# Kernel tuning notes

Measured on AMD Instinct MI355X. Metric: run time of the kernel, lower is better.

## Reference

```python
import jax, jax.numpy as jnp
import numpy as np
from jax import lax

B, T, E, H, D, L = 2048, 512, 128, 8, 16, 3


def _ln(x, g, b):
    m = jnp.mean(x, -1, keepdims=True)
    v = jnp.var(x, -1, keepdims=True)
    return (x - m) / jnp.sqrt(v + 1e-5) * g + b


def _bn(x, g, b):  # eval-mode BatchNorm2d with running_mean=0, running_var=1
    return x * (g / np.sqrt(1.0 + 1e-5))[None, :, None, None] + b[None, :, None, None]


def _conv(x, w, b):  # 3x3 conv, padding=1, NCHW / OIHW
    y = lax.conv_general_dilated(x, w, (1, 1), 'SAME', dimension_numbers=('NCHW', 'OIHW', 'NCHW'))
    return y + b[None, :, None, None]


def _forward(enc_out, x1, x2, x3, c11_w, c11_b, bn11_g, bn11_b, c12_w, c12_b, bn12_g, bn12_b,
             fc1_w, fc1_b, c21_w, c21_b, bn21_g, bn21_b, fc2_w, fc2_b, fc_w, fc_b,
             wk, wq, wv, proj_w, proj_b, ln1_g, ln1_b, ln2_g, ln2_b, ln3_g, ln3_b, ln4_g, ln4_b,
             ff_w1, ff_b1, ff_w2, ff_b2, lnf_g, lnf_b, head_w, head_b):
    # StateNet -> query vector q: [B, E]
    h1 = jax.nn.relu(_bn(_conv(x1, c11_w, c11_b), bn11_g, bn11_b))
    h1 = jax.nn.relu(_bn(_conv(h1, c12_w, c12_b), bn12_g, bn12_b))
    h1 = jax.nn.relu(h1.reshape(h1.shape[0], -1) @ fc1_w + fc1_b)  # [B, 64]
    h2 = jax.nn.relu(_bn(_conv(x2, c21_w, c21_b), bn21_g, bn21_b))
    h2 = jax.nn.relu(h2.reshape(h2.shape[0], -1) @ fc2_w + fc2_b)  # [B, 16]
    q = jax.nn.relu(jnp.concatenate([h1, h2, x3], axis=-1) @ fc_w + fc_b)  # [B, E]

    for l in range(L):  # 3 structurally identical DecoderBlocks
        kx = _ln(enc_out, ln1_g[l], ln1_b[l])
        vx = _ln(enc_out, ln2_g[l], ln2_b[l])
        qx = _ln(q, ln3_g[l], ln3_b[l])
        K = (kx @ wk[l]).reshape(B, T, H, D)
        V = (vx @ wv[l]).reshape(B, T, H, D)
        Q = (qx @ wq[l]).reshape(B, H, D)
        # NOTE: original multiplies (not divides) by head_size**0.5 -- kept faithful.
        wei = jax.nn.softmax(jnp.einsum('bhd,bthd->bht', Q, K) * (D ** 0.5), axis=-1)
        att = jnp.einsum('bht,bthd->bhd', wei, V).reshape(B, E)
        q = q + att @ proj_w[l] + proj_b[l]
        h = _ln(q, ln4_g[l], ln4_b[l])
        q = q + jax.nn.gelu(h @ ff_w1[l] + ff_b1[l], approximate=False) @ ff_w2[l] + ff_b2[l]

    x = _ln(q, lnf_g, lnf_b)
    return x @ head_w + head_b  # discard head logits [B, 37]


def setup_inputs():
    key = jax.random.key(0)
    ks = iter(jax.random.split(key, 32))
    r = lambda *s: jax.random.normal(next(ks), s, jnp.float32) * 0.02
    z = lambda *s: jnp.zeros(s, jnp.float32)
    o = lambda *s: jnp.ones(s, jnp.float32)
    return dict(
        enc_out=jax.random.normal(next(ks), (B, T, E), jnp.float32),
        x1=jax.random.normal(next(ks), (B, 3, 37, 1), jnp.float32),
        x2=jax.random.normal(next(ks), (B, 7, 4, 1), jnp.float32),
        x3=jax.random.normal(next(ks), (B, 4), jnp.float32),
        c11_w=r(8, 3, 3, 3), c11_b=z(8), bn11_g=o(8), bn11_b=z(8),
        c12_w=r(8, 8, 3, 3), c12_b=z(8), bn12_g=o(8), bn12_b=z(8),
        fc1_w=r(296, 64), fc1_b=z(64),
        c21_w=r(8, 7, 3, 3), c21_b=z(8), bn21_g=o(8), bn21_b=z(8),
        fc2_w=r(32, 16), fc2_b=z(16),
        fc_w=r(84, E), fc_b=z(E),
        wk=r(L, E, E), wq=r(L, E, E), wv=r(L, E, E),
        proj_w=r(L, E, E), proj_b=z(L, E),
        ln1_g=o(L, E), ln1_b=z(L, E), ln2_g=o(L, E), ln2_b=z(L, E),
        ln3_g=o(L, E), ln3_b=z(L, E), ln4_g=o(L, E), ln4_b=z(L, E),
        ff_w1=r(L, E, 4 * E), ff_b1=z(L, 4 * E), ff_w2=r(L, 4 * E, E), ff_b2=z(L, E),
        lnf_g=o(E), lnf_b=z(E),
        head_w=r(E, 37), head_b=z(37),
    )


def reference(enc_out, x1, x2, x3, c11_w, c11_b, bn11_g, bn11_b, c12_w, c12_b, bn12_g, bn12_b,
              fc1_w, fc1_b, c21_w, c21_b, bn21_g, bn21_b, fc2_w, fc2_b, fc_w, fc_b,
              wk, wq, wv, proj_w, proj_b, ln1_g, ln1_b, ln2_g, ln2_b, ln3_g, ln3_b, ln4_g, ln4_b,
              ff_w1, ff_b1, ff_w2, ff_b2, lnf_g, lnf_b, head_w, head_b):
    return _forward(enc_out, x1, x2, x3, c11_w, c11_b, bn11_g, bn11_b, c12_w, c12_b, bn12_g, bn12_b,
                    fc1_w, fc1_b, c21_w, c21_b, bn21_g, bn21_b, fc2_w, fc2_b, fc_w, fc_b,
                    wk, wq, wv, proj_w, proj_b, ln1_g, ln1_b, ln2_g, ln2_b, ln3_g, ln3_b, ln4_g, ln4_b,
                    ff_w1, ff_b1, ff_w2, ff_b2, lnf_g, lnf_b, head_w, head_b)
```

## Files before the change

kernel.cpp:

```cpp
#include <hip/hip_runtime.h>
#include <math.h>

typedef unsigned int u32;
typedef unsigned short u16;
typedef unsigned char u8;
typedef __attribute__((ext_vector_type(4))) float f32x4;
typedef __attribute__((ext_vector_type(8))) short bf16x8;

__device__ __forceinline__ u16 f2b(float f){ u32 u=__float_as_uint(f); u=(u+0x7fffu+((u>>16)&1u))>>16; return (u16)u; }
__device__ __forceinline__ float b2f(u16 h){ return __uint_as_float(((u32)h)<<16); }

struct P {
  const float* in[43];
  float* out;
  float* q;
};

__global__ __launch_bounds__(512) void k_state(P p){
  __shared__ float sx1[112];
  __shared__ float sx2[32];
  __shared__ float sa[296];
  __shared__ float sb[296];
  __shared__ float sc2[32];
  __shared__ float sh1[64];
  __shared__ float sh2[16];
  __shared__ float red[512];
  int tid=threadIdx.x; int b=blockIdx.x;
  const float rs_bn = rsqrtf(1.0f+1e-5f);
  const float* x1 = p.in[1] + (size_t)b*111;
  const float* x2 = p.in[2] + (size_t)b*28;
  if (tid<111) sx1[tid]=x1[tid];
  if (tid>=128 && tid<156) sx2[tid-128]=x2[tid-128];
  __syncthreads();
  if (tid<296){
    int cc=tid/37, i=tid-cc*37;
    const float* wgt=p.in[4];
    float acc=p.in[5][cc];
    #pragma unroll
    for(int ic=0;ic<3;++ic)
      #pragma unroll
      for(int kh=0;kh<3;++kh){
        int ii=i+kh-1;
        if((unsigned)ii<37u) acc+=wgt[((cc*3+ic)*3+kh)*3+1]*sx1[ic*37+ii];
      }
    acc=acc*(p.in[6][cc]*rs_bn)+p.in[7][cc];
    sa[tid]=fmaxf(acc,0.f);
  }
  if (tid>=296 && tid<328){
    int o=tid-296, cc=o>>2, i=o&3;
    const float* wgt=p.in[14];
    float acc=p.in[15][cc];
    for(int ic=0;ic<7;++ic)
      for(int kh=0;kh<3;++kh){
        int ii=i+kh-1;
        if((unsigned)ii<4u) acc+=wgt[((cc*7+ic)*3+kh)*3+1]*sx2[ic*4+ii];
      }
    acc=acc*(p.in[16][cc]*rs_bn)+p.in[17][cc];
    sc2[o]=fmaxf(acc,0.f);
  }
  __syncthreads();
  if (tid<296){
    int cc=tid/37, i=tid-cc*37;
    const float* wgt=p.in[8];
    float acc=p.in[9][cc];
    #pragma unroll
    for(int ic=0;ic<8;++ic)
      #pragma unroll
      for(int kh=0;kh<3;++kh){
        int ii=i+kh-1;
        if((unsigned)ii<37u) acc+=wgt[((cc*8+ic)*3+kh)*3+1]*sa[ic*37+ii];
      }
    acc=acc*(p.in[10][cc]*rs_bn)+p.in[11][cc];
    sb[tid]=fmaxf(acc,0.f);
  }
  if (tid>=480 && tid<496){
    int o=tid-480;
    const float* wgt=p.in[18];
    float acc=p.in[19][o];
    for(int k=0;k<32;++k) acc+=sc2[k]*wgt[k*16+o];
    sh2[o]=fmaxf(acc,0.f);
  }
  __syncthreads();
  {
    int o=tid>>3, j=tid&7;
    const float* wgt=p.in[12];
    float part=0.f;
    for(int m=0;m<37;++m){ int k=j*37+m; part+=sb[k]*wgt[k*64+o]; }
    red[o*8+j]=part;
  }
  __syncthreads();
  if (tid<64){
    float acc=p.in[13][tid];
    #pragma unroll
    for(int j=0;j<8;++j) acc+=red[tid*8+j];
    sh1[tid]=fmaxf(acc,0.f);
  }
  __syncthreads();
  if (tid<128){
    const float* wgt=p.in[20];
    const float* x3=p.in[3]+(size_t)b*4;
    float acc=p.in[21][tid];
    for(int k=0;k<64;++k) acc+=sh1[k]*wgt[k*128+tid];
    for(int k=0;k<16;++k) acc+=sh2[k]*wgt[(64+k)*128+tid];
    #pragma unroll
    for(int k=0;k<4;++k) acc+=x3[k]*wgt[(80+k)*128+tid];
    p.q[(size_t)b*128+tid]=fmaxf(acc,0.f);
  }
}

#define FUSED_LDS 157184

__global__ __launch_bounds__(512,1) void k_fused(P p){
  extern __shared__ u8 sm[];
  u16*  XH   = (u16*)sm;
  u8*   WTU  = sm + 139264;
  float* qv   = (float*)(sm + 155904);
  float* wred = (float*)(sm + 156416);
  float* mrow = (float*)(sm + 156928);
  float* invL = (float*)(sm + 156992);
  float* st   = (float*)(sm + 157056);

  float* red  = (float*)(WTU);
  float* qxs  = (float*)(WTU + 2048);
  float* Qs   = (float*)(WTU + 2560);
  u16*  QKb   = (u16*)(WTU + 3072);
  u16*  WT    = (u16*)(WTU);
  float* SS   = (float*)(WTU);
  float* red2 = (float*)(WTU + 4224);
  float* atts = (float*)(WTU + 6272);
  float* qps  = (float*)(WTU + 6784);
  float* qx4  = (float*)(WTU + 7296);
  float* us   = (float*)(WTU + 7808);

  int tid=threadIdx.x;
  int w = tid>>6, lane = tid&63, l15 = lane&15, q4 = lane>>4;
  int b = blockIdx.x;

  {
    const float* enc = p.in[0] + (size_t)b*512*128;
    int g = tid>>5, c = tid&31;
    #pragma unroll 4
    for (int it=0; it<32; ++it){
      int row = it*16 + g;
      float4 v = *(const float4*)(enc + (size_t)row*128 + c*4);
      float s = v.x+v.y+v.z+v.w;
      float s2 = v.x*v.x+v.y*v.y+v.z*v.z+v.w*v.w;
      #pragma unroll
      for (int m=1; m<=16; m<<=1){ s+=__shfl_xor(s,m); s2+=__shfl_xor(s2,m); }
      float mean = s*(1.f/128.f);
      float rstd = rsqrtf(s2*(1.f/128.f)-mean*mean+1e-5f);
      u32 a = (u32)f2b((v.x-mean)*rstd) | ((u32)f2b((v.y-mean)*rstd)<<16);
      u32 bq= (u32)f2b((v.z-mean)*rstd) | ((u32)f2b((v.w-mean)*rstd)<<16);
      *(uint2*)(XH + row*136 + c*4) = make_uint2(a,bq);
    }
    if (tid<128) qv[tid] = p.q[(size_t)b*128 + tid];
  }
  __syncthreads();

  for (int l=0; l<3; ++l){
    const float* wk = p.in[22] + l*16384;
    const float* wq = p.in[23] + l*16384;
    const float* wv = p.in[24] + l*16384;
    const float* pw = p.in[25] + l*16384;
    const float* pb = p.in[26] + l*128;
    const float* g1 = p.in[27] + l*128;
    const float* g2 = p.in[29] + l*128;
    const float* b2v= p.in[30] + l*128;
    const float* g3 = p.in[31] + l*128;
    const float* b3 = p.in[32] + l*128;
    const float* g4 = p.in[33] + l*128;
    const float* b4 = p.in[34] + l*128;
    const float* f1 = p.in[35] + l*65536;
    const float* fb1= p.in[36] + l*512;
    const float* f2 = p.in[37] + l*65536;
    const float* fb2= p.in[38] + l*128;

    if (w==0){
      float x0=qv[lane], x1=qv[lane+64];
      float s=x0+x1, s2=x0*x0+x1*x1;
      #pragma unroll
      for(int m=1;m<=32;m<<=1){ s+=__shfl_xor(s,m); s2+=__shfl_xor(s2,m); }
      if(lane==0){ float mean=s*(1.f/128.f); st[0]=mean; st[1]=rsqrtf(s2*(1.f/128.f)-mean*mean+1e-5f); }
    }
    __syncthreads();
    if (tid<128) qxs[tid]=(qv[tid]-st[0])*st[1]*g3[tid]+b3[tid];
    __syncthreads();

    {
      int o = tid&127, kk = tid>>7;
      float acc=0.f;
      const float* wp = wq + kk*32*128 + o;
      #pragma unroll 8
      for (int e=0;e<32;++e) acc += qxs[kk*32+e]*wp[e*128];
      red[tid]=acc;
    }
    __syncthreads();
    if (tid<128) Qs[tid]=red[tid]+red[tid+128]+red[tid+256]+red[tid+384];
    __syncthreads();

    {
      int h = tid>>5, e0=(tid&31)*4;
      if (h<8){
        float Qh[16];
        #pragma unroll
        for(int d=0;d<16;++d) Qh[d]=Qs[h*16+d];
        #pragma unroll
        for(int j=0;j<4;++j){
          int e=e0+j;
          const float* wr = wk + e*128 + h*16;
          float4 wv0=*(const float4*)(wr), wv1=*(const float4*)(wr+4), wv2=*(const float4*)(wr+8), wv3=*(const float4*)(wr+12);
          float acc = Qh[0]*wv0.x+Qh[1]*wv0.y+Qh[2]*wv0.z+Qh[3]*wv0.w
                    + Qh[4]*wv1.x+Qh[5]*wv1.y+Qh[6]*wv1.z+Qh[7]*wv1.w
                    + Qh[8]*wv2.x+Qh[9]*wv2.y+Qh[10]*wv2.z+Qh[11]*wv2.w
                    + Qh[12]*wv3.x+Qh[13]*wv3.y+Qh[14]*wv3.z+Qh[15]*wv3.w;
          QKb[h*136+e] = f2b(acc*g1[e]*4.f);
        }
      } else {
        #pragma unroll
        for(int j=0;j<4;++j) QKb[h*136+e0+j]=0;
      }
    }
    __syncthreads();

    bf16x8 qkf[4];
    #pragma unroll
    for(int ks=0;ks<4;++ks) qkf[ks]=*(const bf16x8*)(QKb + l15*136 + ks*32 + q4*8);

    f32x4 sc[4];
    #pragma unroll
    for(int mb=0;mb<4;++mb){
      f32x4 c = {0.f,0.f,0.f,0.f};
      #pragma unroll
      for(int ks=0;ks<4;++ks){
        bf16x8 a = *(const bf16x8*)(XH + (64*w + 16*mb + l15)*136 + ks*32 + q4*8);
        c = __builtin_amdgcn_mfma_f32_16x16x32_bf16(a, qkf[ks], c, 0,0,0);
      }
      sc[mb]=c;
    }
    {
      float mx = -INFINITY;
      #pragma unroll
      for(int mb=0;mb<4;++mb)
        #pragma unroll
        for(int r=0;r<4;++r) mx = fmaxf(mx, sc[mb][r]);
      mx = fmaxf(mx, __shfl_xor(mx,16)); mx = fmaxf(mx, __shfl_xor(mx,32));
      if (lane<16) wred[w*16+lane]=mx;
    }
    __syncthreads();
    if (tid<16){
      float m0=wred[tid];
      #pragma unroll
      for(int ww=1;ww<8;++ww) m0=fmaxf(m0, wred[ww*16+tid]);
      mrow[tid]=m0;
    }
    __syncthreads();
    {
      float mh = mrow[l15];
      float ssum=0.f;
      #pragma unroll
      for(int mb=0;mb<4;++mb)
        #pragma unroll
        for(int r=0;r<4;++r){
          int t = 64*w + 16*mb + q4*4 + r;
          float pv = __expf(sc[mb][r]-mh);
          ssum += pv;
          WT[l15*520 + t] = f2b(pv);
        }
      ssum += __shfl_xor(ssum,16); ssum += __shfl_xor(ssum,32);
      if (lane<16) wred[w*16+lane]=ssum;
    }
    __syncthreads();
    if (tid<16) invL[tid] = 1.f/(wred[tid]+wred[16+tid]+wred[32+tid]+wred[48+tid]
                                +wred[64+tid]+wred[80+tid]+wred[96+tid]+wred[112+tid]);
    __syncthreads();

    f32x4 wa = {0.f,0.f,0.f,0.f};
    int eb = w*16 + l15;
    #pragma unroll 4
    for(int ks=0;ks<16;++ks){
      bf16x8 aw = *(const bf16x8*)(WT + l15*520 + ks*32 + q4*8);
      bf16x8 bb;
      #pragma unroll
      for(int j=0;j<8;++j){
        int t = ks*32 + q4*8 + j;
        bb[j] = (short)XH[t*136 + eb];
      }
      wa = __builtin_amdgcn_mfma_f32_16x16x32_bf16(aw, bb, wa, 0,0,0);
    }
    __syncthreads();
    if (q4 < 2){
      float g2e = g2[eb], b2e = b2v[eb];
      #pragma unroll
      for(int r=0;r<4;++r){
        int h = q4*4+r;
        SS[h*132+eb] = wa[r]*invL[h]*g2e + b2e;
      }
    }
    __syncthreads();

    {
      int o = tid&127, kk = tid>>7; int h=o>>4;
      float acc=0.f;
      const float* wp = wv + kk*32*128 + o;
      const float* Sr = SS + h*132 + kk*32;
      #pragma unroll 8
      for(int e=0;e<32;++e) acc += Sr[e]*wp[e*128];
      red2[tid]=acc;
    }
    __syncthreads();
    if (tid<128) atts[tid]=red2[tid]+red2[tid+128]+red2[tid+256]+red2[tid+384];
    __syncthreads();

    {
      int o = tid&127, kk = tid>>7;
      float acc=0.f;
      const float* wp = pw + kk*32*128 + o;
      #pragma unroll 8
      for(int e=0;e<32;++e) acc += atts[kk*32+e]*wp[e*128];
      red2[tid]=acc;
    }
    __syncthreads();
    if (tid<128) qps[tid]= qv[tid] + pb[tid] + red2[tid]+red2[tid+128]+red2[tid+256]+red2[tid+384];
    __syncthreads();

    if (w==0){
      float x0=qps[lane], x1=qps[lane+64];
      float s=x0+x1, s2=x0*x0+x1*x1;
      #pragma unroll
      for(int m=1;m<=32;m<<=1){ s+=__shfl_xor(s,m); s2+=__shfl_xor(s2,m); }
      if(lane==0){ float mean=s*(1.f/128.f); st[0]=mean; st[1]=rsqrtf(s2*(1.f/128.f)-mean*mean+1e-5f); }
    }
    __syncthreads();
    if (tid<128) qx4[tid]=(qps[tid]-st[0])*st[1]*g4[tid]+b4[tid];
    __syncthreads();

    {
      int o = tid;
      float acc=fb1[o];
      const float* wp = f1 + o;
      #pragma unroll 8
      for(int e=0;e<128;++e) acc += qx4[e]*wp[e*512];
      us[o]=0.5f*acc*(1.f+erff(acc*0.70710678118654752f));
    }
    __syncthreads();

    {
      int o = tid&127, kk = tid>>7;
      float acc=0.f;
      const float* wp = f2 + kk*128*128 + o;
      #pragma unroll 8
      for(int e=0;e<128;++e) acc += us[kk*128+e]*wp[e*128];
      red2[tid]=acc;
    }
    __syncthreads();
    if (tid<128) qv[tid]= qps[tid] + fb2[tid] + red2[tid]+red2[tid+128]+red2[tid+256]+red2[tid+384];
    __syncthreads();
  }

  if (w==0){
    float x0=qv[lane], x1=qv[lane+64];
    float s=x0+x1, s2=x0*x0+x1*x1;
    #pragma unroll
    for(int m=1;m<=32;m<<=1){ s+=__shfl_xor(s,m); s2+=__shfl_xor(s2,m); }
    if(lane==0){ float mean=s*(1.f/128.f); st[0]=mean; st[1]=rsqrtf(s2*(1.f/128.f)-mean*mean+1e-5f); }
  }
  __syncthreads();
  if (tid<128) qx4[tid]=(qv[tid]-st[0])*st[1]*p.in[39][tid]+p.in[40][tid];
  __syncthreads();
  if (tid<37){
    const float* hw=p.in[41];
    float acc=p.in[42][tid];
    #pragma unroll 4
    for(int e=0;e<128;++e) acc += qx4[e]*hw[e*37+tid];
    p.out[(size_t)b*37+tid]=acc;
  }
}

extern "C" void kernel_launch(void* const* d_in, const int* in_sizes, int n_in,
                              void* d_out, int out_size, void* d_ws, size_t ws_size,
                              hipStream_t stream) {
  (void)in_sizes; (void)n_in; (void)out_size; (void)ws_size;
  P pa;
  for(int i=0;i<43;++i) pa.in[i]=(const float*)d_in[i];
  pa.out=(float*)d_out;
  pa.q=(float*)d_ws;
  static bool inited=false;
  if (!inited){
    hipFuncSetAttribute(reinterpret_cast<const void*>(k_fused),
                        hipFuncAttributeMaxDynamicSharedMemorySize, FUSED_LDS);
    inited=true;
  }
  k_state<<<2048,512,0,stream>>>(pa);
  k_fused<<<2048,512,FUSED_LDS,stream>>>(pa);
}
```

Baseline: 1.448 ms.

## Double fused block to 1024 threads with split-K reductions and swizzled LDS

Raises the fused decoder kernel from 512 to 1024 threads per block and re-partitions every stage across the extra waves. The GEMVs use 8- or 2-way split-K with LDS reductions, the score MFMA covers 32 rows per wave, and the attention-times-V MFMA splits K across two wave groups that combine partial sums through a new LDS buffer. An XOR swizzle on the LN-normalized encoder tile is meant to reduce LDS bank conflicts on the column-strided reads. The aim is more latency hiding with one block per CU, at the cost of extra reduction traffic and more register pressure under the 1024-thread launch bound.

```diff
diff --git a/kernel.cpp b/kernel.cpp
--- a/kernel.cpp
+++ b/kernel.cpp
@@ -8,7 +8,6 @@
 typedef __attribute__((ext_vector_type(8))) short bf16x8;
 
 __device__ __forceinline__ u16 f2b(float f){ u32 u=__float_as_uint(f); u=(u+0x7fffu+((u>>16)&1u))>>16; return (u16)u; }
-__device__ __forceinline__ float b2f(u16 h){ return __uint_as_float(((u32)h)<<16); }
 
 struct P {
   const float* in[43];
@@ -108,29 +107,41 @@
   }
 }
 
-#define FUSED_LDS 157184
-
-__global__ __launch_bounds__(512,1) void k_fused(P p){
+#define XS 136
+#define WTS 520
+#define SWZ16(r) ((((r)>>3)&3)<<4)
+
+#define O_WTU   139264
+#define O_QV    155904
+#define O_WRED  156416
+#define O_MROW  157440
+#define O_INVL  157504
+#define O_ST    157568
+#define O_PP    157632
+#define FUSED_LDS 161728
+
+__global__ __launch_bounds__(1024,1) void k_fused(P p){
   extern __shared__ u8 sm[];
   u16*  XH   = (u16*)sm;
-  u8*   WTU  = sm + 139264;
-  float* qv   = (float*)(sm + 155904);
-  float* wred = (float*)(sm + 156416);
-  float* mrow = (float*)(sm + 156928);
-  float* invL = (float*)(sm + 156992);
-  float* st   = (float*)(sm + 157056);
+  u8*   WTU  = sm + O_WTU;
+  float* qv   = (float*)(sm + O_QV);
+  float* wred = (float*)(sm + O_WRED);
+  float* mrow = (float*)(sm + O_MROW);
+  float* invL = (float*)(sm + O_INVL);
+  float* st   = (float*)(sm + O_ST);
+  float* PP   = (float*)(sm + O_PP);
 
   float* red  = (float*)(WTU);
-  float* qxs  = (float*)(WTU + 2048);
-  float* Qs   = (float*)(WTU + 2560);
-  u16*  QKb   = (u16*)(WTU + 3072);
+  float* qxs  = (float*)(WTU + 4096);
+  float* Qs   = (float*)(WTU + 4608);
+  u16*  QKb   = (u16*)(WTU + 5120);
   u16*  WT    = (u16*)(WTU);
   float* SS   = (float*)(WTU);
   float* red2 = (float*)(WTU + 4224);
-  float* atts = (float*)(WTU + 6272);
-  float* qps  = (float*)(WTU + 6784);
-  float* qx4  = (float*)(WTU + 7296);
-  float* us   = (float*)(WTU + 7808);
+  float* atts = (float*)(WTU + 8320);
+  float* qps  = (float*)(WTU + 8832);
+  float* qx4  = (float*)(WTU + 9344);
+  float* us   = (float*)(WTU + 9856);
 
   int tid=threadIdx.x;
   int w = tid>>6, lane = tid&63, l15 = lane&15, q4 = lane>>4;
@@ -139,9 +150,9 @@
   {
     const float* enc = p.in[0] + (size_t)b*512*128;
     int g = tid>>5, c = tid&31;
-    #pragma unroll 4
-    for (int it=0; it<32; ++it){
-      int row = it*16 + g;
+    #pragma unroll 8
+    for (int it=0; it<16; ++it){
+      int row = it*32 + g;
       float4 v = *(const float4*)(enc + (size_t)row*128 + c*4);
       float s = v.x+v.y+v.z+v.w;
       float s2 = v.x*v.x+v.y*v.y+v.z*v.z+v.w*v.w;
@@ -151,7 +162,8 @@
       float rstd = rsqrtf(s2*(1.f/128.f)-mean*mean+1e-5f);
       u32 a = (u32)f2b((v.x-mean)*rstd) | ((u32)f2b((v.y-mean)*rstd)<<16);
       u32 bq= (u32)f2b((v.z-mean)*rstd) | ((u32)f2b((v.w-mean)*rstd)<<16);
-      *(uint2*)(XH + row*136 + c*4) = make_uint2(a,bq);
+      int ci = (c*4) ^ SWZ16(row);
+      *(uint2*)(XH + row*XS + ci) = make_uint2(a,bq);
     }
     if (tid<128) qv[tid] = p.q[(size_t)b*128 + tid];
   }
@@ -189,36 +201,36 @@
     {
       int o = tid&127, kk = tid>>7;
       float acc=0.f;
-      const float* wp = wq + kk*32*128 + o;
-      #pragma unroll 8
-      for (int e=0;e<32;++e) acc += qxs[kk*32+e]*wp[e*128];
+      const float* wp = wq + kk*16*128 + o;
+      #pragma unroll
+      for (int e=0;e<16;++e) acc += qxs[kk*16+e]*wp[e*128];
       red[tid]=acc;
     }
     __syncthreads();
-    if (tid<128) Qs[tid]=red[tid]+red[tid+128]+red[tid+256]+red[tid+384];
-    __syncthreads();
-
-    {
-      int h = tid>>5, e0=(tid&31)*4;
-      if (h<8){
-        float Qh[16];
-        #pragma unroll
-        for(int d=0;d<16;++d) Qh[d]=Qs[h*16+d];
-        #pragma unroll
-        for(int j=0;j<4;++j){
-          int e=e0+j;
-          const float* wr = wk + e*128 + h*16;
-          float4 wv0=*(const float4*)(wr), wv1=*(const float4*)(wr+4), wv2=*(const float4*)(wr+8), wv3=*(const float4*)(wr+12);
-          float acc = Qh[0]*wv0.x+Qh[1]*wv0.y+Qh[2]*wv0.z+Qh[3]*wv0.w
-                    + Qh[4]*wv1.x+Qh[5]*wv1.y+Qh[6]*wv1.z+Qh[7]*wv1.w
-                    + Qh[8]*wv2.x+Qh[9]*wv2.y+Qh[10]*wv2.z+Qh[11]*wv2.w
-                    + Qh[12]*wv3.x+Qh[13]*wv3.y+Qh[14]*wv3.z+Qh[15]*wv3.w;
-          QKb[h*136+e] = f2b(acc*g1[e]*4.f);
-        }
-      } else {
-        #pragma unroll
-        for(int j=0;j<4;++j) QKb[h*136+e0+j]=0;
-      }
+    if (tid<128) Qs[tid]=red[tid]+red[tid+128]+red[tid+256]+red[tid+384]
+                        +red[tid+512]+red[tid+640]+red[tid+768]+red[tid+896];
+    __syncthreads();
+
+    if (tid<512){
+      int h = tid>>6, i = tid&63;
+      float Qh[16];
+      #pragma unroll
+      for(int d=0;d<16;++d) Qh[d]=Qs[h*16+d];
+      #pragma unroll
+      for(int j=0;j<2;++j){
+        int e=i*2+j;
+        const float* wr = wk + e*128 + h*16;
+        float4 w0=*(const float4*)(wr), w1=*(const float4*)(wr+4), w2=*(const float4*)(wr+8), w3=*(const float4*)(wr+12);
+        float acc = Qh[0]*w0.x+Qh[1]*w0.y+Qh[2]*w0.z+Qh[3]*w0.w
+                  + Qh[4]*w1.x+Qh[5]*w1.y+Qh[6]*w1.z+Qh[7]*w1.w
+                  + Qh[8]*w2.x+Qh[9]*w2.y+Qh[10]*w2.z+Qh[11]*w2.w
+                  + Qh[12]*w3.x+Qh[13]*w3.y+Qh[14]*w3.z+Qh[15]*w3.w;
+        QKb[h*136+e] = f2b(acc*g1[e]*4.f);
+      }
+    } else if (tid<768){
+      int o=tid-512; int h2=8+(o>>5); int e0=(o&31)*4;
+      #pragma unroll
+      for(int j=0;j<4;++j) QKb[h2*136+e0+j]=0;
     }
     __syncthreads();
 
@@ -226,23 +238,21 @@
     #pragma unroll
     for(int ks=0;ks<4;++ks) qkf[ks]=*(const bf16x8*)(QKb + l15*136 + ks*32 + q4*8);
 
-    f32x4 sc[4];
-    #pragma unroll
-    for(int mb=0;mb<4;++mb){
-      f32x4 c = {0.f,0.f,0.f,0.f};
+    f32x4 sc0={0,0,0,0}, sc1={0,0,0,0};
+    {
+      int r0 = 32*w + l15, r1 = 32*w + 16 + l15;
+      int s0 = SWZ16(r0), s1 = SWZ16(r1);
       #pragma unroll
       for(int ks=0;ks<4;++ks){
-        bf16x8 a = *(const bf16x8*)(XH + (64*w + 16*mb + l15)*136 + ks*32 + q4*8);
-        c = __builtin_amdgcn_mfma_f32_16x16x32_bf16(a, qkf[ks], c, 0,0,0);
-      }
-      sc[mb]=c;
-    }
-    {
-      float mx = -INFINITY;
-      #pragma unroll
-      for(int mb=0;mb<4;++mb)
-        #pragma unroll
-        for(int r=0;r<4;++r) mx = fmaxf(mx, sc[mb][r]);
+        bf16x8 a0 = *(const bf16x8*)(XH + r0*XS + ((ks*32 + q4*8)^s0));
+        bf16x8 a1 = *(const bf16x8*)(XH + r1*XS + ((ks*32 + q4*8)^s1));
+        sc0 = __builtin_amdgcn_mfma_f32_16x16x32_bf16(a0, qkf[ks], sc0, 0,0,0);
+        sc1 = __builtin_amdgcn_mfma_f32_16x16x32_bf16(a1, qkf[ks], sc1, 0,0,0);
+      }
+    }
+    {
+      float mx = fmaxf(fmaxf(fmaxf(sc0[0],sc0[1]),fmaxf(sc0[2],sc0[3])),
+                       fmaxf(fmaxf(sc1[0],sc1[1]),fmaxf(sc1[2],sc1[3])));
       mx = fmaxf(mx, __shfl_xor(mx,16)); mx = fmaxf(mx, __shfl_xor(mx,32));
       if (lane<16) wred[w*16+lane]=mx;
     }
@@ -250,7 +260,7 @@
     if (tid<16){
       float m0=wred[tid];
       #pragma unroll
-      for(int ww=1;ww<8;++ww) m0=fmaxf(m0, wred[ww*16+tid]);
+      for(int ww=1;ww<16;++ww) m0=fmaxf(m0, wred[ww*16+tid]);
       mrow[tid]=m0;
     }
     __syncthreads();
@@ -258,42 +268,51 @@
       float mh = mrow[l15];
       float ssum=0.f;
       #pragma unroll
-      for(int mb=0;mb<4;++mb)
-        #pragma unroll
-        for(int r=0;r<4;++r){
-          int t = 64*w + 16*mb + q4*4 + r;
-          float pv = __expf(sc[mb][r]-mh);
-          ssum += pv;
-          WT[l15*520 + t] = f2b(pv);
-        }
+      for(int r=0;r<4;++r){
+        int t0 = 32*w + q4*4 + r;
+        float p0 = __expf(sc0[r]-mh);
+        float p1 = __expf(sc1[r]-mh);
+        WT[l15*WTS + t0]      = f2b(p0);
+        WT[l15*WTS + t0 + 16] = f2b(p1);
+        ssum += p0+p1;
+      }
       ssum += __shfl_xor(ssum,16); ssum += __shfl_xor(ssum,32);
       if (lane<16) wred[w*16+lane]=ssum;
     }
     __syncthreads();
-    if (tid<16) invL[tid] = 1.f/(wred[tid]+wred[16+tid]+wred[32+tid]+wred[48+tid]
-                                +wred[64+tid]+wred[80+tid]+wred[96+tid]+wred[112+tid]);
+    if (tid<16){
+      float s0=0.f;
+      #pragma unroll
+      for(int ww=0;ww<16;++ww) s0+=wred[ww*16+tid];
+      invL[tid] = 1.f/s0;
+    }
     __syncthreads();
 
     f32x4 wa = {0.f,0.f,0.f,0.f};
-    int eb = w*16 + l15;
-    #pragma unroll 4
-    for(int ks=0;ks<16;++ks){
-      bf16x8 aw = *(const bf16x8*)(WT + l15*520 + ks*32 + q4*8);
+    int wp8 = w&7, ksb = (w>>3)*8;
+    int eb  = wp8*16 + l15;
+    int ebs = eb ^ (q4<<4);
+    #pragma unroll
+    for(int kss=0;kss<8;++kss){
+      int ks = ksb + kss;
+      bf16x8 aw = *(const bf16x8*)(WT + l15*WTS + ks*32 + q4*8);
       bf16x8 bb;
       #pragma unroll
       for(int j=0;j<8;++j){
         int t = ks*32 + q4*8 + j;
-        bb[j] = (short)XH[t*136 + eb];
+        bb[j] = (short)XH[t*XS + ebs];
       }
       wa = __builtin_amdgcn_mfma_f32_16x16x32_bf16(aw, bb, wa, 0,0,0);
     }
-    __syncthreads();
-    if (q4 < 2){
+    if (w>=8 && q4<2) *(f32x4*)(PP + ((w-8)*32 + q4*16 + l15)*4) = wa;
+    __syncthreads();
+    if (w<8 && q4<2){
+      f32x4 pp = *(const f32x4*)(PP + (w*32 + q4*16 + l15)*4);
       float g2e = g2[eb], b2e = b2v[eb];
       #pragma unroll
       for(int r=0;r<4;++r){
         int h = q4*4+r;
-        SS[h*132+eb] = wa[r]*invL[h]*g2e + b2e;
+        SS[h*132+eb] = (wa[r]+pp[r])*invL[h]*g2e + b2e;
       }
     }
     __syncthreads();
@@ -301,26 +320,29 @@
     {
       int o = tid&127, kk = tid>>7; int h=o>>4;
       float acc=0.f;
-      const float* wp = wv + kk*32*128 + o;
-      const float* Sr = SS + h*132 + kk*32;
-      #pragma unroll 8
-      for(int e=0;e<32;++e) acc += Sr[e]*wp[e*128];
+      const float* wp = wv + kk*16*128 + o;
+      const float* Sr = SS + h*132 + kk*16;
+      #pragma unroll
+      for(int e=0;e<16;++e) acc += Sr[e]*wp[e*128];
       red2[tid]=acc;
     }
     __syncthreads();
-    if (tid<128) atts[tid]=red2[tid]+red2[tid+128]+red2[tid+256]+red2[tid+384];
+    if (tid<128) atts[tid]=red2[tid]+red2[tid+128]+red2[tid+256]+red2[tid+384]
+                          +red2[tid+512]+red2[tid+640]+red2[tid+768]+red2[tid+896];
     __syncthreads();
 
     {
       int o = tid&127, kk = tid>>7;
       float acc=0.f;
-      const float* wp = pw + kk*32*128 + o;
-      #pragma unroll 8
-      for(int e=0;e<32;++e) acc += atts[kk*32+e]*wp[e*128];
+      const float* wp = pw + kk*16*128 + o;
+      #pragma unroll
+      for(int e=0;e<16;++e) acc += atts[kk*16+e]*wp[e*128];
       red2[tid]=acc;
     }
     __syncthreads();
-    if (tid<128) qps[tid]= qv[tid] + pb[tid] + red2[tid]+red2[tid+128]+red2[tid+256]+red2[tid+384];
+    if (tid<128) qps[tid]= qv[tid] + pb[tid]
+                          + red2[tid]+red2[tid+128]+red2[tid+256]+red2[tid+384]
+                          + red2[tid+512]+red2[tid+640]+red2[tid+768]+red2[tid+896];
     __syncthreads();
 
     if (w==0){
@@ -335,25 +357,32 @@
     __syncthreads();
 
     {
-      int o = tid;
-      float acc=fb1[o];
-      const float* wp = f1 + o;
-      #pragma unroll 8
-      for(int e=0;e<128;++e) acc += qx4[e]*wp[e*512];
-      us[o]=0.5f*acc*(1.f+erff(acc*0.70710678118654752f));
+      int o = tid&511, kk = tid>>9;
+      float acc=0.f;
+      const float* wp = f1 + (size_t)kk*64*512 + o;
+      #pragma unroll 16
+      for(int e=0;e<64;++e) acc += qx4[kk*64+e]*wp[e*512];
+      red2[tid]=acc;
+    }
+    __syncthreads();
+    if (tid<512){
+      float u=red2[tid]+red2[tid+512]+fb1[tid];
+      us[tid]=0.5f*u*(1.f+erff(u*0.70710678118654752f));
     }
     __syncthreads();
 
     {
       int o = tid&127, kk = tid>>7;
       float acc=0.f;
-      const float* wp = f2 + kk*128*128 + o;
-      #pragma unroll 8
-      for(int e=0;e<128;++e) acc += us[kk*128+e]*wp[e*128];
+      const float* wp = f2 + (size_t)kk*64*128 + o;
+      #pragma unroll 16
+      for(int e=0;e<64;++e) acc += us[kk*64+e]*wp[e*128];
       red2[tid]=acc;
     }
     __syncthreads();
-    if (tid<128) qv[tid]= qps[tid] + fb2[tid] + red2[tid]+red2[tid+128]+red2[tid+256]+red2[tid+384];
+    if (tid<128) qv[tid]= qps[tid] + fb2[tid]
+                         + red2[tid]+red2[tid+128]+red2[tid+256]+red2[tid+384]
+                         + red2[tid+512]+red2[tid+640]+red2[tid+768]+red2[tid+896];
     __syncthreads();
   }
 
@@ -370,7 +399,7 @@
   if (tid<37){
     const float* hw=p.in[41];
     float acc=p.in[42][tid];
-    #pragma unroll 4
+    #pragma unroll 8
     for(int e=0;e<128;++e) acc += qx4[e]*hw[e*37+tid];
     p.out[(size_t)b*37+tid]=acc;
   }
@@ -391,5 +420,5 @@
     inited=true;
   }
   k_state<<<2048,512,0,stream>>>(pa);
-  k_fused<<<2048,512,FUSED_LDS,stream>>>(pa);
+  k_fused<<<2048,1024,FUSED_LDS,stream>>>(pa);
 }
```

Result: slower. 1.974 ms (+36.4%).
